# Optimization experiments

Hardware: AMD Instinct MI355X
Metric: run time of the kernel (lower is better)

Reference implementation:

```python
import jax, jax.numpy as jnp
import numpy as np

SIZE = 896   # hidden_size
HALF = 448   # hidden_size // 2
BINS = 256   # 2 ** (bits / 2)
B, T = 32, 1024


def _scale(x):
    # [0, BINS-1] ints -> [-1, 1] floats
    return x.astype(jnp.float32) / ((BINS - 1) / 2.0) - 1.0


def _reorder(w):
    # torch GRU layout (r, u, e) each split coarse/fine ->
    # (coarse_r, coarse_u, coarse_e, fine_r, fine_u, fine_e)
    cr, fr, cu, fu, ce, fe = jnp.split(w, 6, axis=0)
    return jnp.concatenate([cr, cu, ce, fr, fu, fe], axis=0)


def setup_inputs():
    key = jax.random.key(0)
    ks = jax.random.split(key, 14)
    s = 0.05
    return {
        'conditional': jax.random.normal(ks[0], (B, 3 * SIZE, T), jnp.float32) * s,
        'w_coarse_in': jax.random.normal(ks[1], (3 * HALF, 2), jnp.float32) * s,
        'w_fine_in': jax.random.normal(ks[2], (3 * HALF, 3), jnp.float32) * s,
        'w_hh': jax.random.normal(ks[3], (3 * SIZE, SIZE), jnp.float32) * s,
        'b_ih': jax.random.normal(ks[4], (3 * SIZE,), jnp.float32) * s,
        'b_hh': jax.random.normal(ks[5], (3 * SIZE,), jnp.float32) * s,
        'wc1': jax.random.normal(ks[6], (HALF, HALF), jnp.float32) * s,
        'bc1': jax.random.normal(ks[7], (HALF,), jnp.float32) * s,
        'wc2': jax.random.normal(ks[8], (BINS, HALF), jnp.float32) * s,
        'bc2': jax.random.normal(ks[9], (BINS,), jnp.float32) * s,
        'wf1': jax.random.normal(ks[10], (HALF, HALF), jnp.float32) * s,
        'bf1': jax.random.normal(ks[11], (HALF,), jnp.float32) * s,
        'wf2': jax.random.normal(ks[12], (BINS, HALF), jnp.float32) * s,
        'bf2': jax.random.normal(ks[13], (BINS,), jnp.float32) * s,
    }


def _gru_softmax_step(hid, ip, hp, W1, b1, W2, b2):
    # hid: [HALF, B]; ip, hp: [3*HALF, B]
    ru = jax.nn.sigmoid(hp[:2 * HALF] + ip[:2 * HALF])
    r, u = ru[:HALF], ru[HALF:]
    e = jnp.tanh(r * hp[2 * HALF:] + ip[2 * HALF:])
    hid = u * hid + (1.0 - u) * e
    h = jax.nn.relu(hid.T @ W1.T + b1)          # [B, HALF]
    logits = h @ W2.T + b2                       # [B, BINS]
    sample = jnp.argmax(logits, axis=1).astype(jnp.int32)  # argmax=True path
    return hid, sample


def reference(conditional, w_coarse_in, w_fine_in, w_hh, b_ih, b_hh,
              wc1, bc1, wc2, bc2, wf1, bf1, wf2, bf2):
    batch, _, sig_len = conditional.shape
    # [B, 3*SIZE, T] -> [B, T, 3, SIZE], add input bias, split coarse/fine halves
    cond = conditional.transpose(0, 2, 1).reshape(batch, sig_len, 3, SIZE)
    g = cond + b_ih.reshape(3, SIZE)
    # reshape keeps gate order (r, u, e) concatenated along last dim
    bias_c = g[..., :HALF].reshape(batch, sig_len, 3 * HALF).transpose(1, 2, 0)  # [T, 3H, B]
    bias_f = g[..., HALF:].reshape(batch, sig_len, 3 * HALF).transpose(1, 2, 0)

    w_hh_r = _reorder(w_hh)                 # [3*SIZE, SIZE]
    b_hh_r = _reorder(b_hh[:, None])        # [3*SIZE, 1]

    def step(carry, xs):
        coarse, fine, c_hid, f_hid = carry
        bc, bf = xs
        hidden = jnp.concatenate([c_hid, f_hid], axis=0)        # [SIZE, B]
        hp = w_hh_r @ hidden + b_hh_r                            # [3*SIZE, B]
        hp_c, hp_f = hp[:3 * HALF], hp[3 * HALF:]
        cin = jnp.stack([_scale(coarse), _scale(fine)], axis=1)  # [B, 2]
        c_hid, new_coarse = _gru_softmax_step(
            c_hid, w_coarse_in @ cin.T + bc, hp_c, wc1, bc1, wc2, bc2)
        fin = jnp.stack([_scale(coarse), _scale(fine), _scale(new_coarse)], axis=1)  # [B, 3]
        f_hid, new_fine = _gru_softmax_step(
            f_hid, w_fine_in @ fin.T + bf, hp_f, wf1, bf1, wf2, bf2)
        return (new_coarse, new_fine, c_hid, f_hid), (new_coarse, new_fine)

    init = (jnp.full((batch,), BINS // 2, jnp.int32),   # go coarse sample
            jnp.zeros((batch,), jnp.int32),              # go fine sample
            jnp.zeros((HALF, batch), jnp.float32),
            jnp.zeros((HALF, batch), jnp.float32))
    carry, (oc, of) = jax.lax.scan(step, init, (bias_c, bias_f))
    final_hidden = jnp.concatenate([carry[2], carry[3]], axis=0)  # [SIZE, B]
    return oc.T, of.T, final_hidden
```

## Files before the change

### kernel.cpp

```cpp
#include <hip/hip_runtime.h>
#include <math.h>


#define HALFN  448
#define SIZEN  896
#define RTOT   2688
#define NB     32
#define TSTEPS 1024
#define NWG    224
#define NTHR   512
#define CONDSTR (RTOT * TSTEPS)
#define RBN    28
#define FANIN  28

#define OFF_HID0  0
#define OFF_HID1  28672
#define OFF_H1TC  57344
#define OFF_H1TF  71680
#define OFF_NCP   86016
#define OFF_NFP   86080
#define OFF_DCTRC 86144
#define OFF_DCTRF 86176
#define OFF_FLAGS 86208

typedef unsigned long long u64t;

__device__ __forceinline__ int orig_row(int r) {
  int c = r / HALFN, o = r - c * HALFN;
  int oc = (c < 3) ? (2 * c) : (2 * (c - 3) + 1);
  return oc * HALFN + o;
}
__device__ __forceinline__ float sigm(float x) { return 1.0f / (1.0f + expf(-x)); }

__device__ __forceinline__ float gload(const float* p) {
  return __hip_atomic_load(const_cast<float*>(p), __ATOMIC_RELAXED, __HIP_MEMORY_SCOPE_AGENT);
}
__device__ __forceinline__ void gstore(float* p, float v) {
  __hip_atomic_store(p, v, __ATOMIC_RELAXED, __HIP_MEMORY_SCOPE_AGENT);
}
__device__ __forceinline__ u64t gload64(const u64t* p) {
  return __hip_atomic_load(const_cast<u64t*>(p), __ATOMIC_RELAXED, __HIP_MEMORY_SCOPE_AGENT);
}
__device__ __forceinline__ void gstore64(u64t* p, u64t v) {
  __hip_atomic_store(p, v, __ATOMIC_RELAXED, __HIP_MEMORY_SCOPE_AGENT);
}
__device__ __forceinline__ void gmax64(u64t* p, u64t v) {
  __hip_atomic_fetch_max(p, v, __ATOMIC_RELAXED, __HIP_MEMORY_SCOPE_AGENT);
}
__device__ __forceinline__ unsigned ctrload(const unsigned* p) {
  return __hip_atomic_load(const_cast<unsigned*>(p), __ATOMIC_RELAXED, __HIP_MEMORY_SCOPE_AGENT);
}
__device__ __forceinline__ unsigned f2ord(float f) {
  unsigned u = __float_as_uint(f);
  return (u & 0x80000000u) ? ~u : (u | 0x80000000u);
}

struct __align__(16) SM {
  float whh[12][SIZEN];
  float wc1l[2][HALFN];
  float wf1l[2][HALFN];
  float wc2l[10][HALFN];
  float wf2l[10][HALFN];
  float red[8][12][32];
  float condw[12][16][33];
  float h1c4[4][HALFN];
  float fcr[4][16][8];
  float flog[4][16];
  float hps[6][32];
  float hpfl[6][32];
  float chid[2][32];
  float fhid[2][32];
  float scvo[32], sfvo[32], sncn[32];
  float ncraw[32], nfraw[32];
  float wcil[2][3][2];
  float wfil[2][3][3];
  float bihl[12];
  float bhh_l[12];
  float bc2l[10], bf2l[10];
};

__device__ __forceinline__ void gridbar(unsigned* flags, unsigned ep, int& dead) {
  asm volatile("s_waitcnt vmcnt(0)" ::: "memory");
  __syncthreads();
  if (threadIdx.x == 0)
    __hip_atomic_store(&flags[blockIdx.x], ep, __ATOMIC_RELAXED, __HIP_MEMORY_SCOPE_AGENT);
  if (!dead) {
    int iters = 0;
    for (;;) {
      int ok = 1;
      if (threadIdx.x < NWG) {
        unsigned v = __hip_atomic_load(&flags[threadIdx.x], __ATOMIC_RELAXED, __HIP_MEMORY_SCOPE_AGENT);
        ok = (v >= ep) ? 1 : 0;
      }
      if (__syncthreads_and(ok)) break;
      if (++iters > (1 << 20)) { dead = 1; break; }
      __builtin_amdgcn_s_sleep(1);
    }
  } else {
    __syncthreads();
  }
}

__device__ __forceinline__ void pollmany(unsigned* arr, int n, unsigned target, int& dead) {
  if (!dead) {
    int it = 0;
    for (;;) {
      int ok = 1;
      if ((int)threadIdx.x < n)
        ok = (ctrload(&arr[threadIdx.x]) >= target) ? 1 : 0;
      if (__syncthreads_and(ok)) break;
      if (++it > (1 << 20)) { dead = 1; break; }
      __builtin_amdgcn_s_sleep(1);
    }
  } else {
    __syncthreads();
  }
}

extern "C" __global__ void wavernn_init(float* ws) {
  int i = blockIdx.x * blockDim.x + threadIdx.x;
  int st = gridDim.x * blockDim.x;
  for (int k = i; k < 2 * SIZEN * NB; k += st) ws[k] = 0.0f;
  if (i < 64) ((u64t*)(ws + OFF_NCP))[i] = 0ull;
  if (i < 64) ((unsigned*)(ws + OFF_DCTRC))[i] = 0u;
  if (i < 256) ((unsigned*)(ws + OFF_FLAGS))[i] = 0u;
}

extern "C" __global__ void __launch_bounds__(NTHR)
wavernn_persist(const float* __restrict__ cond,
                const float* __restrict__ wci, const float* __restrict__ wfi,
                const float* __restrict__ whh, const float* __restrict__ bih,
                const float* __restrict__ bhh,
                const float* __restrict__ wc1, const float* __restrict__ bc1,
                const float* __restrict__ wc2, const float* __restrict__ bc2,
                const float* __restrict__ wf1, const float* __restrict__ bf1,
                const float* __restrict__ wf2, const float* __restrict__ bf2,
                float* __restrict__ out, float* ws) {
  __shared__ SM sm;

  float* hid0 = ws + OFF_HID0;
  float* hid1 = ws + OFF_HID1;
  float* h1tc = ws + OFF_H1TC;
  float* h1tf = ws + OFF_H1TF;
  u64t*  ncp  = (u64t*)(ws + OFF_NCP);
  u64t*  nfp  = (u64t*)(ws + OFF_NFP);
  unsigned* dctrc = (unsigned*)(ws + OFF_DCTRC);
  unsigned* dctrf = (unsigned*)(ws + OFF_DCTRF);
  unsigned* flags = (unsigned*)(ws + OFF_FLAGS);

  const int w = blockIdx.x, tid = threadIdx.x;
  const int b = tid & 31, ks = tid >> 5;
  const int rb = w >> 3, bg = w & 7;
  const int fc2start = (rb < 4) ? rb * 10 : 40 + (rb - 4) * 9;
  const int fc2len   = (rb < 4) ? 10 : 9;
  unsigned ep = 0;
  int dead = 0;

#pragma unroll
  for (int rr = 0; rr < 12; rr++) {
    int R = (rr >> 1) * HALFN + 2 * w + (rr & 1);
    const float* src = whh + (size_t)orig_row(R) * SIZEN;
    for (int k = tid * 4; k < SIZEN; k += NTHR * 4)
      *(float4*)&sm.whh[rr][k] = *(const float4*)&src[k];
  }
  if (tid < 12) sm.bhh_l[tid] = bhh[orig_row((tid >> 1) * HALFN + 2 * w + (tid & 1))];
  for (int k = tid * 4; k < HALFN; k += NTHR * 4) {
    *(float4*)&sm.wc1l[0][k] = *(const float4*)&wc1[(size_t)(2 * w) * HALFN + k];
    *(float4*)&sm.wc1l[1][k] = *(const float4*)&wc1[(size_t)(2 * w + 1) * HALFN + k];
    *(float4*)&sm.wf1l[0][k] = *(const float4*)&wf1[(size_t)(2 * w) * HALFN + k];
    *(float4*)&sm.wf1l[1][k] = *(const float4*)&wf1[(size_t)(2 * w + 1) * HALFN + k];
  }
  for (int rr = 0; rr < fc2len; rr++) {
    for (int k = tid * 4; k < HALFN; k += NTHR * 4) {
      *(float4*)&sm.wc2l[rr][k] = *(const float4*)&wc2[(size_t)(fc2start + rr) * HALFN + k];
      *(float4*)&sm.wf2l[rr][k] = *(const float4*)&wf2[(size_t)(fc2start + rr) * HALFN + k];
    }
  }
  if (tid < fc2len) { sm.bc2l[tid] = bc2[fc2start + tid]; sm.bf2l[tid] = bf2[fc2start + tid]; }
  if (tid < 12) {
    int rk = tid;
    int R = ((rk >= 6) ? HALFN : 0) + ((rk % 6) >> 1) * SIZEN + 2 * w + (rk & 1);
    sm.bihl[rk] = bih[R];
  }
  if (tid < 2) {
    int j = 2 * w + tid;
#pragma unroll
    for (int g = 0; g < 3; g++) {
      sm.wcil[tid][g][0] = wci[(g * HALFN + j) * 2 + 0];
      sm.wcil[tid][g][1] = wci[(g * HALFN + j) * 2 + 1];
      sm.wfil[tid][g][0] = wfi[(g * HALFN + j) * 3 + 0];
      sm.wfil[tid][g][1] = wfi[(g * HALFN + j) * 3 + 1];
      sm.wfil[tid][g][2] = wfi[(g * HALFN + j) * 3 + 2];
    }
  }
  if (tid < 64) { sm.chid[tid >> 5][tid & 31] = 0.0f; sm.fhid[tid >> 5][tid & 31] = 0.0f; }
  if (tid < 32) { sm.scvo[tid] = 128.0f * (2.0f / 255.0f) - 1.0f; sm.sfvo[tid] = -1.0f; }
  __syncthreads();

  for (int t = 0; t < TSTEPS; ++t) {
    const float* hprev = (t & 1) ? hid0 : hid1;
    float*       hcur  = (t & 1) ? hid1 : hid0;
    const int tt = t & 15;

    {
      if (tt == 0) {
        for (int idx = tid; idx < 1536; idx += NTHR) {
          int rk = idx >> 7, rem = idx & 127;
          int bb = rem >> 2, part = rem & 3;
          int R = ((rk >= 6) ? HALFN : 0) + ((rk % 6) >> 1) * SIZEN + 2 * w + (rk & 1);
          float4 v = *(const float4*)&cond[(size_t)bb * CONDSTR + (size_t)R * TSTEPS + t + part * 4];
          sm.condw[rk][part * 4 + 0][bb] = v.x;
          sm.condw[rk][part * 4 + 1][bb] = v.y;
          sm.condw[rk][part * 4 + 2][bb] = v.z;
          sm.condw[rk][part * 4 + 3][bb] = v.w;
        }
      }

      float acc[12];
#pragma unroll
      for (int rr = 0; rr < 12; rr++) acc[rr] = 0.0f;
      const int k0 = ks * 56;
      const float* hcol = hprev + b;
#pragma unroll 2
      for (int k = k0; k < k0 + 56; k += 4) {
        float h0 = gload(&hcol[(k + 0) * 32]), h1v = gload(&hcol[(k + 1) * 32]);
        float h2 = gload(&hcol[(k + 2) * 32]), h3  = gload(&hcol[(k + 3) * 32]);
#pragma unroll
        for (int rr = 0; rr < 12; rr++) {
          const float4 wv = *(const float4*)&sm.whh[rr][k];
          acc[rr] = fmaf(wv.x, h0, fmaf(wv.y, h1v, fmaf(wv.z, h2, fmaf(wv.w, h3, acc[rr]))));
        }
      }
#pragma unroll
      for (int rr = 0; rr < 12; rr++) acc[rr] += __shfl_xor(acc[rr], 32);
      __syncthreads();
      if ((tid & 32) == 0) {
        int slot = ks >> 1;
#pragma unroll
        for (int rr = 0; rr < 12; rr++) sm.red[slot][rr][b] = acc[rr];
      }
      __syncthreads();
      if (tid < 384) {
        int rr = tid >> 5, bb = tid & 31;
        float s = sm.bhh_l[rr];
#pragma unroll
        for (int kk = 0; kk < 8; kk++) s += sm.red[kk][rr][bb];
        if (rr < 6) sm.hps[rr][bb] = s;
        else        sm.hpfl[rr - 6][bb] = s;
      }
      if (t > 0) {
        pollmany(dctrf, 32, FANIN * (unsigned)t, dead);
        if (tid < 32) {
          u64t p = gload64(&nfp[tid]);
          unsigned nf = 0xFFFFFFFFu - (unsigned)(p & 0xFFFFFFFFull);
          sm.sfvo[tid] = (float)nf * (2.0f / 255.0f) - 1.0f;
          sm.nfraw[tid] = (float)nf;
        }
      }
      __syncthreads();
      if (t > 0 && w < 32 && tid == 64)
        out[32768 + (size_t)w * TSTEPS + (t - 1)] = sm.nfraw[w];
      if (tid < 64) {
        int q = tid >> 5, bb = tid & 31;
        float sc = sm.scvo[bb], sf = sm.sfvo[bb];
        float ipr = sm.wcil[q][0][0] * sc + sm.wcil[q][0][1] * sf + sm.condw[0 + q][tt][bb] + sm.bihl[0 + q];
        float ipu = sm.wcil[q][1][0] * sc + sm.wcil[q][1][1] * sf + sm.condw[2 + q][tt][bb] + sm.bihl[2 + q];
        float ipe = sm.wcil[q][2][0] * sc + sm.wcil[q][2][1] * sf + sm.condw[4 + q][tt][bb] + sm.bihl[4 + q];
        float r = sigm(sm.hps[0 + q][bb] + ipr);
        float u = sigm(sm.hps[2 + q][bb] + ipu);
        float e = tanhf(fmaf(r, sm.hps[4 + q][bb], ipe));
        float hnew = u * sm.chid[q][bb] + (1.0f - u) * e;
        sm.chid[q][bb] = hnew;
        gstore(&hcur[(size_t)(2 * w + q) * 32 + bb], hnew);
      }
    }
    gridbar(flags, ++ep, dead);

    {
      const int k0 = ks * 28;
      float a0 = 0.0f, a1 = 0.0f;
      const float* hcc = hcur + b;
#pragma unroll
      for (int k = k0; k < k0 + 28; k += 4) {
        float h0 = gload(&hcc[(k + 0) * 32]), h1v = gload(&hcc[(k + 1) * 32]);
        float h2 = gload(&hcc[(k + 2) * 32]), h3  = gload(&hcc[(k + 3) * 32]);
        float4 v0 = *(const float4*)&sm.wc1l[0][k];
        a0 = fmaf(v0.x, h0, fmaf(v0.y, h1v, fmaf(v0.z, h2, fmaf(v0.w, h3, a0))));
        float4 v1 = *(const float4*)&sm.wc1l[1][k];
        a1 = fmaf(v1.x, h0, fmaf(v1.y, h1v, fmaf(v1.z, h2, fmaf(v1.w, h3, a1))));
      }
      a0 += __shfl_xor(a0, 32); a1 += __shfl_xor(a1, 32);
      __syncthreads();
      if ((tid & 32) == 0) { sm.red[ks >> 1][0][b] = a0; sm.red[ks >> 1][1][b] = a1; }
      if (w < 32 && tid == 256) gstore64(&nfp[w], 0ull);
      __syncthreads();
      if (tid < 64) {
        int rr = tid >> 5, bb = tid & 31;
        float s = bc1[2 * w + rr];
#pragma unroll
        for (int kk = 0; kk < 8; kk++) s += sm.red[kk][rr][bb];
        gstore(&h1tc[(size_t)bb * HALFN + 2 * w + rr], fmaxf(s, 0.0f));
      }
    }
    gridbar(flags, ++ep, dead);

    {
#pragma unroll
      for (int bq = 0; bq < 4; bq++)
        if (tid < HALFN) sm.h1c4[bq][tid] = gload(&h1tc[(size_t)(4 * bg + bq) * HALFN + tid]);
      __syncthreads();
      {
        int bq = tid >> 7, rl = (tid >> 3) & 15, kss = tid & 7;
        if (rl < fc2len) {
          const float* wrow = sm.wc2l[rl];
          const float* hcol = sm.h1c4[bq];
          float a = 0.0f;
          int kk0 = kss * 56;
#pragma unroll
          for (int k = kk0; k < kk0 + 56; k += 4) {
            float4 wv = *(const float4*)&wrow[k];
            float4 hv = *(const float4*)&hcol[k];
            a = fmaf(wv.x, hv.x, fmaf(wv.y, hv.y, fmaf(wv.z, hv.z, fmaf(wv.w, hv.w, a))));
          }
          sm.fcr[bq][rl][kss] = a;
        }
      }
      __syncthreads();
      if (tid < 64) {
        int bq = tid >> 4, rl = tid & 15;
        if (rl < fc2len) {
          float s = sm.bc2l[rl];
#pragma unroll
          for (int q = 0; q < 8; q++) s += sm.fcr[bq][rl][q];
          sm.flog[bq][rl] = s;
        }
      }
      __syncthreads();
      if (tid < 4) {
        int bq = tid;
        float bv = sm.flog[bq][0]; int bi = 0;
        for (int rl = 1; rl < fc2len; rl++) {
          float x = sm.flog[bq][rl];
          if (x > bv) { bv = x; bi = rl; }
        }
        u64t pack = ((u64t)f2ord(bv) << 32) | (u64t)(0xFFFFFFFFu - (unsigned)(fc2start + bi));
        gmax64(&ncp[4 * bg + bq], pack);
        asm volatile("s_waitcnt vmcnt(0)" ::: "memory");
        __hip_atomic_fetch_add(&dctrc[4 * bg + bq], 1u, __ATOMIC_RELAXED, __HIP_MEMORY_SCOPE_AGENT);
      }
    }
    pollmany(dctrc, 32, FANIN * (unsigned)(t + 1), dead);

    {
      if (tid < 32) {
        u64t p = gload64(&ncp[tid]);
        unsigned nc = 0xFFFFFFFFu - (unsigned)(p & 0xFFFFFFFFull);
        sm.sncn[tid] = (float)nc * (2.0f / 255.0f) - 1.0f;
        sm.ncraw[tid] = (float)nc;
      }
      __syncthreads();
      if (w < 32 && tid == 64) out[(size_t)w * TSTEPS + t] = sm.ncraw[w];
      if (tid < 64) {
        int q = tid >> 5, bb = tid & 31;
        float sc = sm.scvo[bb], sf = sm.sfvo[bb], snc = sm.sncn[bb];
        float ipr = sm.wfil[q][0][0] * sc + sm.wfil[q][0][1] * sf + sm.wfil[q][0][2] * snc
                  + sm.condw[6 + q][tt][bb] + sm.bihl[6 + q];
        float ipu = sm.wfil[q][1][0] * sc + sm.wfil[q][1][1] * sf + sm.wfil[q][1][2] * snc
                  + sm.condw[8 + q][tt][bb] + sm.bihl[8 + q];
        float ipe = sm.wfil[q][2][0] * sc + sm.wfil[q][2][1] * sf + sm.wfil[q][2][2] * snc
                  + sm.condw[10 + q][tt][bb] + sm.bihl[10 + q];
        float r = sigm(sm.hpfl[0 + q][bb] + ipr);
        float u = sigm(sm.hpfl[2 + q][bb] + ipu);
        float e = tanhf(fmaf(r, sm.hpfl[4 + q][bb], ipe));
        float hnew = u * sm.fhid[q][bb] + (1.0f - u) * e;
        sm.fhid[q][bb] = hnew;
        gstore(&hcur[(size_t)(HALFN + 2 * w + q) * 32 + bb], hnew);
      }
      __syncthreads();
      if (tid < 32) sm.scvo[tid] = sm.sncn[tid];
    }
    gridbar(flags, ++ep, dead);

    {
      const int k0 = ks * 28;
      float a0 = 0.0f, a1 = 0.0f;
      const float* hff = hcur + HALFN * 32 + b;
#pragma unroll
      for (int k = k0; k < k0 + 28; k += 4) {
        float h0 = gload(&hff[(k + 0) * 32]), h1v = gload(&hff[(k + 1) * 32]);
        float h2 = gload(&hff[(k + 2) * 32]), h3  = gload(&hff[(k + 3) * 32]);
        float4 v0 = *(const float4*)&sm.wf1l[0][k];
        a0 = fmaf(v0.x, h0, fmaf(v0.y, h1v, fmaf(v0.z, h2, fmaf(v0.w, h3, a0))));
        float4 v1 = *(const float4*)&sm.wf1l[1][k];
        a1 = fmaf(v1.x, h0, fmaf(v1.y, h1v, fmaf(v1.z, h2, fmaf(v1.w, h3, a1))));
      }
      a0 += __shfl_xor(a0, 32); a1 += __shfl_xor(a1, 32);
      __syncthreads();
      if ((tid & 32) == 0) { sm.red[ks >> 1][0][b] = a0; sm.red[ks >> 1][1][b] = a1; }
      if (w < 32 && tid == 256) gstore64(&ncp[w], 0ull);
      __syncthreads();
      if (tid < 64) {
        int rr = tid >> 5, bb = tid & 31;
        float s = bf1[2 * w + rr];
#pragma unroll
        for (int kk = 0; kk < 8; kk++) s += sm.red[kk][rr][bb];
        gstore(&h1tf[(size_t)bb * HALFN + 2 * w + rr], fmaxf(s, 0.0f));
      }
    }
    gridbar(flags, ++ep, dead);

    {
#pragma unroll
      for (int bq = 0; bq < 4; bq++)
        if (tid < HALFN) sm.h1c4[bq][tid] = gload(&h1tf[(size_t)(4 * bg + bq) * HALFN + tid]);
      __syncthreads();
      {
        int bq = tid >> 7, rl = (tid >> 3) & 15, kss = tid & 7;
        if (rl < fc2len) {
          const float* wrow = sm.wf2l[rl];
          const float* hcol = sm.h1c4[bq];
          float a = 0.0f;
          int kk0 = kss * 56;
#pragma unroll
          for (int k = kk0; k < kk0 + 56; k += 4) {
            float4 wv = *(const float4*)&wrow[k];
            float4 hv = *(const float4*)&hcol[k];
            a = fmaf(wv.x, hv.x, fmaf(wv.y, hv.y, fmaf(wv.z, hv.z, fmaf(wv.w, hv.w, a))));
          }
          sm.fcr[bq][rl][kss] = a;
        }
      }
      __syncthreads();
      if (tid < 64) {
        int bq = tid >> 4, rl = tid & 15;
        if (rl < fc2len) {
          float s = sm.bf2l[rl];
#pragma unroll
          for (int q = 0; q < 8; q++) s += sm.fcr[bq][rl][q];
          sm.flog[bq][rl] = s;
        }
      }
      __syncthreads();
      if (tid < 4) {
        int bq = tid;
        float bv = sm.flog[bq][0]; int bi = 0;
        for (int rl = 1; rl < fc2len; rl++) {
          float x = sm.flog[bq][rl];
          if (x > bv) { bv = x; bi = rl; }
        }
        u64t pack = ((u64t)f2ord(bv) << 32) | (u64t)(0xFFFFFFFFu - (unsigned)(fc2start + bi));
        gmax64(&nfp[4 * bg + bq], pack);
        asm volatile("s_waitcnt vmcnt(0)" ::: "memory");
        __hip_atomic_fetch_add(&dctrf[4 * bg + bq], 1u, __ATOMIC_RELAXED, __HIP_MEMORY_SCOPE_AGENT);
      }
    }
  }

  pollmany(dctrf, 32, FANIN * (unsigned)TSTEPS, dead);
  if (w < 32 && tid == 0) {
    u64t p = gload64(&nfp[w]);
    unsigned nf = 0xFFFFFFFFu - (unsigned)(p & 0xFFFFFFFFull);
    out[32768 + (size_t)w * TSTEPS + (TSTEPS - 1)] = (float)nf;
  }
  if (tid < 64) {
    int q = tid >> 5, bb = tid & 31;
    out[65536 + (size_t)(2 * w + q) * 32 + bb]         = sm.chid[q][bb];
    out[65536 + (size_t)(HALFN + 2 * w + q) * 32 + bb] = sm.fhid[q][bb];
  }
}

extern "C" void kernel_launch(void* const* d_in, const int* in_sizes, int n_in,
                              void* d_out, int out_size, void* d_ws, size_t ws_size,
                              hipStream_t stream) {
  const float* cond = (const float*)d_in[0];
  const float* wci  = (const float*)d_in[1];
  const float* wfi  = (const float*)d_in[2];
  const float* whh  = (const float*)d_in[3];
  const float* bih  = (const float*)d_in[4];
  const float* bhh  = (const float*)d_in[5];
  const float* wc1  = (const float*)d_in[6];
  const float* bc1  = (const float*)d_in[7];
  const float* wc2  = (const float*)d_in[8];
  const float* bc2  = (const float*)d_in[9];
  const float* wf1  = (const float*)d_in[10];
  const float* bf1  = (const float*)d_in[11];
  const float* wf2  = (const float*)d_in[12];
  const float* bf2  = (const float*)d_in[13];
  float* out = (float*)d_out;
  float* ws  = (float*)d_ws;

  hipLaunchKernelGGL(wavernn_init, dim3(64), dim3(256), 0, stream, ws);
  hipLaunchKernelGGL(wavernn_persist, dim3(NWG), dim3(NTHR), 0, stream,
                     cond, wci, wfi, whh, bih, bhh,
                     wc1, bc1, wc2, bc2, wf1, bf1, wf2, bf2, out, ws);
}
```

Before: 31.50 ms.

## Overlap next-step hidden matvec with fine-sample wait and shrink barrier polling to one wave

Moves the recurrent W_hh·h matvec for step t+1 to the end of step t, right after the fine-GRU hidden update, so it runs before the poll for the fine sample instead of sitting on the critical path after it. The coarse-input partial sum that does not depend on the fine sample is also precomputed. Grid barrier and counter polling now use a single wave with __all instead of block-wide __syncthreads_and, and the FC2 weight rows in shared memory are padded to avoid LDS bank conflicts. This relies on the hidden state being complete for all workgroups before the next-step matvec starts, and it makes the control flow more complex.

```diff
diff --git a/kernel.cpp b/kernel.cpp
--- a/kernel.cpp
+++ b/kernel.cpp
@@ -10,8 +10,8 @@
 #define NWG    224
 #define NTHR   512
 #define CONDSTR (RTOT * TSTEPS)
-#define RBN    28
 #define FANIN  28
+#define FC2PAD 452
 
 #define OFF_HID0  0
 #define OFF_HID1  28672
@@ -59,8 +59,8 @@
   float whh[12][SIZEN];
   float wc1l[2][HALFN];
   float wf1l[2][HALFN];
-  float wc2l[10][HALFN];
-  float wf2l[10][HALFN];
+  float wc2l[10][FC2PAD];
+  float wf2l[10][FC2PAD];
   float red[8][12][32];
   float condw[12][16][33];
   float h1c4[4][HALFN];
@@ -68,6 +68,7 @@
   float flog[4][16];
   float hps[6][32];
   float hpfl[6][32];
+  float ip0c[6][32];
   float chid[2][32];
   float fhid[2][32];
   float scvo[32], sfvo[32], sncn[32];
@@ -84,37 +85,39 @@
   __syncthreads();
   if (threadIdx.x == 0)
     __hip_atomic_store(&flags[blockIdx.x], ep, __ATOMIC_RELAXED, __HIP_MEMORY_SCOPE_AGENT);
-  if (!dead) {
-    int iters = 0;
-    for (;;) {
-      int ok = 1;
-      if (threadIdx.x < NWG) {
-        unsigned v = __hip_atomic_load(&flags[threadIdx.x], __ATOMIC_RELAXED, __HIP_MEMORY_SCOPE_AGENT);
-        ok = (v >= ep) ? 1 : 0;
-      }
-      if (__syncthreads_and(ok)) break;
-      if (++iters > (1 << 20)) { dead = 1; break; }
-      __builtin_amdgcn_s_sleep(1);
-    }
-  } else {
-    __syncthreads();
-  }
-}
-
-__device__ __forceinline__ void pollmany(unsigned* arr, int n, unsigned target, int& dead) {
-  if (!dead) {
+  if (threadIdx.x < 64 && !dead) {
     int it = 0;
     for (;;) {
       int ok = 1;
-      if ((int)threadIdx.x < n)
-        ok = (ctrload(&arr[threadIdx.x]) >= target) ? 1 : 0;
-      if (__syncthreads_and(ok)) break;
+#pragma unroll
+      for (int q = 0; q < 4; q++) {
+        int idx = (int)threadIdx.x + q * 64;
+        if (idx < NWG) {
+          unsigned v = __hip_atomic_load(&flags[idx], __ATOMIC_RELAXED, __HIP_MEMORY_SCOPE_AGENT);
+          ok &= (v >= ep) ? 1 : 0;
+        }
+      }
+      if (__all(ok)) break;
       if (++it > (1 << 20)) { dead = 1; break; }
       __builtin_amdgcn_s_sleep(1);
     }
-  } else {
-    __syncthreads();
-  }
+  }
+  __syncthreads();
+}
+
+__device__ __forceinline__ void pollmany(unsigned* arr, unsigned target, int& dead) {
+  if (threadIdx.x < 64 && !dead) {
+    int it = 0;
+    for (;;) {
+      int ok = 1;
+      if (threadIdx.x < 32)
+        ok = (ctrload(&arr[threadIdx.x]) >= target) ? 1 : 0;
+      if (__all(ok)) break;
+      if (++it > (1 << 20)) { dead = 1; break; }
+      __builtin_amdgcn_s_sleep(1);
+    }
+  }
+  __syncthreads();
 }
 
 extern "C" __global__ void wavernn_init(float* ws) {
@@ -197,59 +200,40 @@
   if (tid < 32) { sm.scvo[tid] = 128.0f * (2.0f / 255.0f) - 1.0f; sm.sfvo[tid] = -1.0f; }
   __syncthreads();
 
+  {
+    for (int idx = tid; idx < 1536; idx += NTHR) {
+      int rk = idx >> 7, rem = idx & 127;
+      int bb = rem >> 2, part = rem & 3;
+      int R = ((rk >= 6) ? HALFN : 0) + ((rk % 6) >> 1) * SIZEN + 2 * w + (rk & 1);
+      float4 v = *(const float4*)&cond[(size_t)bb * CONDSTR + (size_t)R * TSTEPS + 0 + part * 4];
+      sm.condw[rk][part * 4 + 0][bb] = v.x;
+      sm.condw[rk][part * 4 + 1][bb] = v.y;
+      sm.condw[rk][part * 4 + 2][bb] = v.z;
+      sm.condw[rk][part * 4 + 3][bb] = v.w;
+    }
+    __syncthreads();
+    if (tid < 384) {
+      int rr = tid >> 5, bb = tid & 31;
+      float s = sm.bhh_l[rr];
+      if (rr < 6) sm.hps[rr][bb] = s;
+      else        sm.hpfl[rr - 6][bb] = s;
+    }
+    if (tid < 192) {
+      int g2 = tid >> 5, bb = tid & 31;
+      int q = g2 & 1, g = g2 >> 1;
+      sm.ip0c[g2][bb] = sm.wcil[q][g][0] * sm.scvo[bb] + sm.condw[g2][0][bb] + sm.bihl[g2];
+    }
+    __syncthreads();
+  }
+
   for (int t = 0; t < TSTEPS; ++t) {
-    const float* hprev = (t & 1) ? hid0 : hid1;
+    const float* hcurG = (t & 1) ? hid1 : hid0;
     float*       hcur  = (t & 1) ? hid1 : hid0;
     const int tt = t & 15;
 
     {
-      if (tt == 0) {
-        for (int idx = tid; idx < 1536; idx += NTHR) {
-          int rk = idx >> 7, rem = idx & 127;
-          int bb = rem >> 2, part = rem & 3;
-          int R = ((rk >= 6) ? HALFN : 0) + ((rk % 6) >> 1) * SIZEN + 2 * w + (rk & 1);
-          float4 v = *(const float4*)&cond[(size_t)bb * CONDSTR + (size_t)R * TSTEPS + t + part * 4];
-          sm.condw[rk][part * 4 + 0][bb] = v.x;
-          sm.condw[rk][part * 4 + 1][bb] = v.y;
-          sm.condw[rk][part * 4 + 2][bb] = v.z;
-          sm.condw[rk][part * 4 + 3][bb] = v.w;
-        }
-      }
-
-      float acc[12];
-#pragma unroll
-      for (int rr = 0; rr < 12; rr++) acc[rr] = 0.0f;
-      const int k0 = ks * 56;
-      const float* hcol = hprev + b;
-#pragma unroll 2
-      for (int k = k0; k < k0 + 56; k += 4) {
-        float h0 = gload(&hcol[(k + 0) * 32]), h1v = gload(&hcol[(k + 1) * 32]);
-        float h2 = gload(&hcol[(k + 2) * 32]), h3  = gload(&hcol[(k + 3) * 32]);
-#pragma unroll
-        for (int rr = 0; rr < 12; rr++) {
-          const float4 wv = *(const float4*)&sm.whh[rr][k];
-          acc[rr] = fmaf(wv.x, h0, fmaf(wv.y, h1v, fmaf(wv.z, h2, fmaf(wv.w, h3, acc[rr]))));
-        }
-      }
-#pragma unroll
-      for (int rr = 0; rr < 12; rr++) acc[rr] += __shfl_xor(acc[rr], 32);
-      __syncthreads();
-      if ((tid & 32) == 0) {
-        int slot = ks >> 1;
-#pragma unroll
-        for (int rr = 0; rr < 12; rr++) sm.red[slot][rr][b] = acc[rr];
-      }
-      __syncthreads();
-      if (tid < 384) {
-        int rr = tid >> 5, bb = tid & 31;
-        float s = sm.bhh_l[rr];
-#pragma unroll
-        for (int kk = 0; kk < 8; kk++) s += sm.red[kk][rr][bb];
-        if (rr < 6) sm.hps[rr][bb] = s;
-        else        sm.hpfl[rr - 6][bb] = s;
-      }
       if (t > 0) {
-        pollmany(dctrf, 32, FANIN * (unsigned)t, dead);
+        pollmany(dctrf, FANIN * (unsigned)t, dead);
         if (tid < 32) {
           u64t p = gload64(&nfp[tid]);
           unsigned nf = 0xFFFFFFFFu - (unsigned)(p & 0xFFFFFFFFull);
@@ -262,10 +246,10 @@
         out[32768 + (size_t)w * TSTEPS + (t - 1)] = sm.nfraw[w];
       if (tid < 64) {
         int q = tid >> 5, bb = tid & 31;
-        float sc = sm.scvo[bb], sf = sm.sfvo[bb];
-        float ipr = sm.wcil[q][0][0] * sc + sm.wcil[q][0][1] * sf + sm.condw[0 + q][tt][bb] + sm.bihl[0 + q];
-        float ipu = sm.wcil[q][1][0] * sc + sm.wcil[q][1][1] * sf + sm.condw[2 + q][tt][bb] + sm.bihl[2 + q];
-        float ipe = sm.wcil[q][2][0] * sc + sm.wcil[q][2][1] * sf + sm.condw[4 + q][tt][bb] + sm.bihl[4 + q];
+        float sf = sm.sfvo[bb];
+        float ipr = sm.ip0c[0 + q][bb] + sm.wcil[q][0][1] * sf;
+        float ipu = sm.ip0c[2 + q][bb] + sm.wcil[q][1][1] * sf;
+        float ipe = sm.ip0c[4 + q][bb] + sm.wcil[q][2][1] * sf;
         float r = sigm(sm.hps[0 + q][bb] + ipr);
         float u = sigm(sm.hps[2 + q][bb] + ipu);
         float e = tanhf(fmaf(r, sm.hps[4 + q][bb], ipe));
@@ -349,7 +333,7 @@
         __hip_atomic_fetch_add(&dctrc[4 * bg + bq], 1u, __ATOMIC_RELAXED, __HIP_MEMORY_SCOPE_AGENT);
       }
     }
-    pollmany(dctrc, 32, FANIN * (unsigned)(t + 1), dead);
+    pollmany(dctrc, FANIN * (unsigned)(t + 1), dead);
 
     {
       if (tid < 32) {
@@ -454,9 +438,63 @@
         __hip_atomic_fetch_add(&dctrf[4 * bg + bq], 1u, __ATOMIC_RELAXED, __HIP_MEMORY_SCOPE_AGENT);
       }
     }
-  }
-
-  pollmany(dctrf, 32, FANIN * (unsigned)TSTEPS, dead);
+
+    if (t + 1 < TSTEPS) {
+      const int tn = t + 1, ttn = tn & 15;
+      if (ttn == 0) {
+        __syncthreads();
+        for (int idx = tid; idx < 1536; idx += NTHR) {
+          int rk = idx >> 7, rem = idx & 127;
+          int bb = rem >> 2, part = rem & 3;
+          int R = ((rk >= 6) ? HALFN : 0) + ((rk % 6) >> 1) * SIZEN + 2 * w + (rk & 1);
+          float4 v = *(const float4*)&cond[(size_t)bb * CONDSTR + (size_t)R * TSTEPS + tn + part * 4];
+          sm.condw[rk][part * 4 + 0][bb] = v.x;
+          sm.condw[rk][part * 4 + 1][bb] = v.y;
+          sm.condw[rk][part * 4 + 2][bb] = v.z;
+          sm.condw[rk][part * 4 + 3][bb] = v.w;
+        }
+      }
+      float acc[12];
+#pragma unroll
+      for (int rr = 0; rr < 12; rr++) acc[rr] = 0.0f;
+      const int k0 = ks * 56;
+      const float* hcol = hcurG + b;
+#pragma unroll 2
+      for (int k = k0; k < k0 + 56; k += 4) {
+        float h0 = gload(&hcol[(k + 0) * 32]), h1v = gload(&hcol[(k + 1) * 32]);
+        float h2 = gload(&hcol[(k + 2) * 32]), h3  = gload(&hcol[(k + 3) * 32]);
+#pragma unroll
+        for (int rr = 0; rr < 12; rr++) {
+          const float4 wv = *(const float4*)&sm.whh[rr][k];
+          acc[rr] = fmaf(wv.x, h0, fmaf(wv.y, h1v, fmaf(wv.z, h2, fmaf(wv.w, h3, acc[rr]))));
+        }
+      }
+#pragma unroll
+      for (int rr = 0; rr < 12; rr++) acc[rr] += __shfl_xor(acc[rr], 32);
+      __syncthreads();
+      if ((tid & 32) == 0) {
+        int slot = ks >> 1;
+#pragma unroll
+        for (int rr = 0; rr < 12; rr++) sm.red[slot][rr][b] = acc[rr];
+      }
+      __syncthreads();
+      if (tid < 384) {
+        int rr = tid >> 5, bb = tid & 31;
+        float s = sm.bhh_l[rr];
+#pragma unroll
+        for (int kk = 0; kk < 8; kk++) s += sm.red[kk][rr][bb];
+        if (rr < 6) sm.hps[rr][bb] = s;
+        else        sm.hpfl[rr - 6][bb] = s;
+      }
+      if (tid < 192) {
+        int g2 = tid >> 5, bb = tid & 31;
+        int q = g2 & 1, g = g2 >> 1;
+        sm.ip0c[g2][bb] = sm.wcil[q][g][0] * sm.scvo[bb] + sm.condw[g2][ttn][bb] + sm.bihl[g2];
+      }
+    }
+  }
+
+  pollmany(dctrf, FANIN * (unsigned)TSTEPS, dead);
   if (w < 32 && tid == 0) {
     u64t p = gload64(&nfp[w]);
     unsigned nf = 0xFFFFFFFFu - (unsigned)(p & 0xFFFFFFFFull);
```

New measurement: 33.13 ms. 1.05x slower.

## Double workgroup threads, halve per-thread K slices, single-wave barrier polling

Applied to the files above, without the earlier changes.

Raises the persistent kernel's block size from 512 to 1024 threads. Each thread now handles 28-element K slices in the recurrent matvec and the output-layer dot products, with 16-way reductions instead of 8. To make room in LDS, the second-layer weights and biases are no longer cached in shared memory and are read from global memory instead. Grid barriers and counter polls now spin in a single wave using __all instead of block-wide __syncthreads_and, which cuts per-iteration polling sync cost but adds global weight reads on the fc2 path.

```diff
diff --git a/kernel.cpp b/kernel.cpp
--- a/kernel.cpp
+++ b/kernel.cpp
@@ -8,9 +8,8 @@
 #define NB     32
 #define TSTEPS 1024
 #define NWG    224
-#define NTHR   512
+#define NTHR   1024
 #define CONDSTR (RTOT * TSTEPS)
-#define RBN    28
 #define FANIN  28
 
 #define OFF_HID0  0
@@ -59,12 +58,10 @@
   float whh[12][SIZEN];
   float wc1l[2][HALFN];
   float wf1l[2][HALFN];
-  float wc2l[10][HALFN];
-  float wf2l[10][HALFN];
-  float red[8][12][32];
+  float red[16][12][32];
   float condw[12][16][33];
   float h1c4[4][HALFN];
-  float fcr[4][16][8];
+  float fcr[4][16][16];
   float flog[4][16];
   float hps[6][32];
   float hpfl[6][32];
@@ -76,7 +73,6 @@
   float wfil[2][3][3];
   float bihl[12];
   float bhh_l[12];
-  float bc2l[10], bf2l[10];
 };
 
 __device__ __forceinline__ void gridbar(unsigned* flags, unsigned ep, int& dead) {
@@ -84,37 +80,39 @@
   __syncthreads();
   if (threadIdx.x == 0)
     __hip_atomic_store(&flags[blockIdx.x], ep, __ATOMIC_RELAXED, __HIP_MEMORY_SCOPE_AGENT);
-  if (!dead) {
-    int iters = 0;
-    for (;;) {
-      int ok = 1;
-      if (threadIdx.x < NWG) {
-        unsigned v = __hip_atomic_load(&flags[threadIdx.x], __ATOMIC_RELAXED, __HIP_MEMORY_SCOPE_AGENT);
-        ok = (v >= ep) ? 1 : 0;
-      }
-      if (__syncthreads_and(ok)) break;
-      if (++iters > (1 << 20)) { dead = 1; break; }
-      __builtin_amdgcn_s_sleep(1);
-    }
-  } else {
-    __syncthreads();
-  }
-}
-
-__device__ __forceinline__ void pollmany(unsigned* arr, int n, unsigned target, int& dead) {
-  if (!dead) {
+  if (threadIdx.x < 64 && !dead) {
     int it = 0;
     for (;;) {
       int ok = 1;
-      if ((int)threadIdx.x < n)
-        ok = (ctrload(&arr[threadIdx.x]) >= target) ? 1 : 0;
-      if (__syncthreads_and(ok)) break;
+#pragma unroll
+      for (int q = 0; q < 4; q++) {
+        int idx = (int)threadIdx.x + q * 64;
+        if (idx < NWG) {
+          unsigned v = __hip_atomic_load(&flags[idx], __ATOMIC_RELAXED, __HIP_MEMORY_SCOPE_AGENT);
+          ok &= (v >= ep) ? 1 : 0;
+        }
+      }
+      if (__all(ok)) break;
       if (++it > (1 << 20)) { dead = 1; break; }
       __builtin_amdgcn_s_sleep(1);
     }
-  } else {
-    __syncthreads();
-  }
+  }
+  __syncthreads();
+}
+
+__device__ __forceinline__ void pollmany(unsigned* arr, unsigned target, int& dead) {
+  if (threadIdx.x < 64 && !dead) {
+    int it = 0;
+    for (;;) {
+      int ok = 1;
+      if (threadIdx.x < 32)
+        ok = (ctrload(&arr[threadIdx.x]) >= target) ? 1 : 0;
+      if (__all(ok)) break;
+      if (++it > (1 << 20)) { dead = 1; break; }
+      __builtin_amdgcn_s_sleep(1);
+    }
+  }
+  __syncthreads();
 }
 
 extern "C" __global__ void wavernn_init(float* ws) {
@@ -170,13 +168,6 @@
     *(float4*)&sm.wf1l[0][k] = *(const float4*)&wf1[(size_t)(2 * w) * HALFN + k];
     *(float4*)&sm.wf1l[1][k] = *(const float4*)&wf1[(size_t)(2 * w + 1) * HALFN + k];
   }
-  for (int rr = 0; rr < fc2len; rr++) {
-    for (int k = tid * 4; k < HALFN; k += NTHR * 4) {
-      *(float4*)&sm.wc2l[rr][k] = *(const float4*)&wc2[(size_t)(fc2start + rr) * HALFN + k];
-      *(float4*)&sm.wf2l[rr][k] = *(const float4*)&wf2[(size_t)(fc2start + rr) * HALFN + k];
-    }
-  }
-  if (tid < fc2len) { sm.bc2l[tid] = bc2[fc2start + tid]; sm.bf2l[tid] = bf2[fc2start + tid]; }
   if (tid < 12) {
     int rk = tid;
     int R = ((rk >= 6) ? HALFN : 0) + ((rk % 6) >> 1) * SIZEN + 2 * w + (rk & 1);
@@ -219,10 +210,10 @@
       float acc[12];
 #pragma unroll
       for (int rr = 0; rr < 12; rr++) acc[rr] = 0.0f;
-      const int k0 = ks * 56;
+      const int k0 = ks * 28;
       const float* hcol = hprev + b;
-#pragma unroll 2
-      for (int k = k0; k < k0 + 56; k += 4) {
+#pragma unroll
+      for (int k = k0; k < k0 + 28; k += 4) {
         float h0 = gload(&hcol[(k + 0) * 32]), h1v = gload(&hcol[(k + 1) * 32]);
         float h2 = gload(&hcol[(k + 2) * 32]), h3  = gload(&hcol[(k + 3) * 32]);
 #pragma unroll
@@ -244,12 +235,12 @@
         int rr = tid >> 5, bb = tid & 31;
         float s = sm.bhh_l[rr];
 #pragma unroll
-        for (int kk = 0; kk < 8; kk++) s += sm.red[kk][rr][bb];
+        for (int kk = 0; kk < 16; kk++) s += sm.red[kk][rr][bb];
         if (rr < 6) sm.hps[rr][bb] = s;
         else        sm.hpfl[rr - 6][bb] = s;
       }
       if (t > 0) {
-        pollmany(dctrf, 32, FANIN * (unsigned)t, dead);
+        pollmany(dctrf, FANIN * (unsigned)t, dead);
         if (tid < 32) {
           u64t p = gload64(&nfp[tid]);
           unsigned nf = 0xFFFFFFFFu - (unsigned)(p & 0xFFFFFFFFull);
@@ -277,22 +268,24 @@
     gridbar(flags, ++ep, dead);
 
     {
-      const int k0 = ks * 28;
       float a0 = 0.0f, a1 = 0.0f;
-      const float* hcc = hcur + b;
-#pragma unroll
-      for (int k = k0; k < k0 + 28; k += 4) {
-        float h0 = gload(&hcc[(k + 0) * 32]), h1v = gload(&hcc[(k + 1) * 32]);
-        float h2 = gload(&hcc[(k + 2) * 32]), h3  = gload(&hcc[(k + 3) * 32]);
-        float4 v0 = *(const float4*)&sm.wc1l[0][k];
-        a0 = fmaf(v0.x, h0, fmaf(v0.y, h1v, fmaf(v0.z, h2, fmaf(v0.w, h3, a0))));
-        float4 v1 = *(const float4*)&sm.wc1l[1][k];
-        a1 = fmaf(v1.x, h0, fmaf(v1.y, h1v, fmaf(v1.z, h2, fmaf(v1.w, h3, a1))));
-      }
-      a0 += __shfl_xor(a0, 32); a1 += __shfl_xor(a1, 32);
-      __syncthreads();
-      if ((tid & 32) == 0) { sm.red[ks >> 1][0][b] = a0; sm.red[ks >> 1][1][b] = a1; }
-      if (w < 32 && tid == 256) gstore64(&nfp[w], 0ull);
+      if (ks < 16) {
+        const int k0 = ks * 28;
+        const float* hcc = hcur + b;
+#pragma unroll
+        for (int k = k0; k < k0 + 28; k += 4) {
+          float h0 = gload(&hcc[(k + 0) * 32]), h1v = gload(&hcc[(k + 1) * 32]);
+          float h2 = gload(&hcc[(k + 2) * 32]), h3  = gload(&hcc[(k + 3) * 32]);
+          float4 v0 = *(const float4*)&sm.wc1l[0][k];
+          a0 = fmaf(v0.x, h0, fmaf(v0.y, h1v, fmaf(v0.z, h2, fmaf(v0.w, h3, a0))));
+          float4 v1 = *(const float4*)&sm.wc1l[1][k];
+          a1 = fmaf(v1.x, h0, fmaf(v1.y, h1v, fmaf(v1.z, h2, fmaf(v1.w, h3, a1))));
+        }
+        a0 += __shfl_xor(a0, 32); a1 += __shfl_xor(a1, 32);
+      }
+      __syncthreads();
+      if (ks < 16 && (tid & 32) == 0) { sm.red[ks >> 1][0][b] = a0; sm.red[ks >> 1][1][b] = a1; }
+      if (w < 32 && tid == 512) gstore64(&nfp[w], 0ull);
       __syncthreads();
       if (tid < 64) {
         int rr = tid >> 5, bb = tid & 31;
@@ -305,19 +298,18 @@
     gridbar(flags, ++ep, dead);
 
     {
-#pragma unroll
-      for (int bq = 0; bq < 4; bq++)
-        if (tid < HALFN) sm.h1c4[bq][tid] = gload(&h1tc[(size_t)(4 * bg + bq) * HALFN + tid]);
+      for (int i = tid; i < 4 * HALFN; i += NTHR)
+        sm.h1c4[i / HALFN][i % HALFN] = gload(&h1tc[(size_t)(4 * bg + i / HALFN) * HALFN + (i % HALFN)]);
       __syncthreads();
       {
-        int bq = tid >> 7, rl = (tid >> 3) & 15, kss = tid & 7;
+        int bq = tid >> 8, rl = (tid >> 4) & 15, kss = tid & 15;
         if (rl < fc2len) {
-          const float* wrow = sm.wc2l[rl];
+          const float* wrow = wc2 + (size_t)(fc2start + rl) * HALFN;
           const float* hcol = sm.h1c4[bq];
           float a = 0.0f;
-          int kk0 = kss * 56;
-#pragma unroll
-          for (int k = kk0; k < kk0 + 56; k += 4) {
+          int kk0 = kss * 28;
+#pragma unroll
+          for (int k = kk0; k < kk0 + 28; k += 4) {
             float4 wv = *(const float4*)&wrow[k];
             float4 hv = *(const float4*)&hcol[k];
             a = fmaf(wv.x, hv.x, fmaf(wv.y, hv.y, fmaf(wv.z, hv.z, fmaf(wv.w, hv.w, a))));
@@ -329,9 +321,9 @@
       if (tid < 64) {
         int bq = tid >> 4, rl = tid & 15;
         if (rl < fc2len) {
-          float s = sm.bc2l[rl];
-#pragma unroll
-          for (int q = 0; q < 8; q++) s += sm.fcr[bq][rl][q];
+          float s = bc2[fc2start + rl];
+#pragma unroll
+          for (int q = 0; q < 16; q++) s += sm.fcr[bq][rl][q];
           sm.flog[bq][rl] = s;
         }
       }
@@ -349,7 +341,7 @@
         __hip_atomic_fetch_add(&dctrc[4 * bg + bq], 1u, __ATOMIC_RELAXED, __HIP_MEMORY_SCOPE_AGENT);
       }
     }
-    pollmany(dctrc, 32, FANIN * (unsigned)(t + 1), dead);
+    pollmany(dctrc, FANIN * (unsigned)(t + 1), dead);
 
     {
       if (tid < 32) {
@@ -382,22 +374,24 @@
     gridbar(flags, ++ep, dead);
 
     {
-      const int k0 = ks * 28;
       float a0 = 0.0f, a1 = 0.0f;
-      const float* hff = hcur + HALFN * 32 + b;
-#pragma unroll
-      for (int k = k0; k < k0 + 28; k += 4) {
-        float h0 = gload(&hff[(k + 0) * 32]), h1v = gload(&hff[(k + 1) * 32]);
-        float h2 = gload(&hff[(k + 2) * 32]), h3  = gload(&hff[(k + 3) * 32]);
-        float4 v0 = *(const float4*)&sm.wf1l[0][k];
-        a0 = fmaf(v0.x, h0, fmaf(v0.y, h1v, fmaf(v0.z, h2, fmaf(v0.w, h3, a0))));
-        float4 v1 = *(const float4*)&sm.wf1l[1][k];
-        a1 = fmaf(v1.x, h0, fmaf(v1.y, h1v, fmaf(v1.z, h2, fmaf(v1.w, h3, a1))));
-      }
-      a0 += __shfl_xor(a0, 32); a1 += __shfl_xor(a1, 32);
-      __syncthreads();
-      if ((tid & 32) == 0) { sm.red[ks >> 1][0][b] = a0; sm.red[ks >> 1][1][b] = a1; }
-      if (w < 32 && tid == 256) gstore64(&ncp[w], 0ull);
+      if (ks < 16) {
+        const int k0 = ks * 28;
+        const float* hff = hcur + HALFN * 32 + b;
+#pragma unroll
+        for (int k = k0; k < k0 + 28; k += 4) {
+          float h0 = gload(&hff[(k + 0) * 32]), h1v = gload(&hff[(k + 1) * 32]);
+          float h2 = gload(&hff[(k + 2) * 32]), h3  = gload(&hff[(k + 3) * 32]);
+          float4 v0 = *(const float4*)&sm.wf1l[0][k];
+          a0 = fmaf(v0.x, h0, fmaf(v0.y, h1v, fmaf(v0.z, h2, fmaf(v0.w, h3, a0))));
+          float4 v1 = *(const float4*)&sm.wf1l[1][k];
+          a1 = fmaf(v1.x, h0, fmaf(v1.y, h1v, fmaf(v1.z, h2, fmaf(v1.w, h3, a1))));
+        }
+        a0 += __shfl_xor(a0, 32); a1 += __shfl_xor(a1, 32);
+      }
+      __syncthreads();
+      if (ks < 16 && (tid & 32) == 0) { sm.red[ks >> 1][0][b] = a0; sm.red[ks >> 1][1][b] = a1; }
+      if (w < 32 && tid == 512) gstore64(&ncp[w], 0ull);
       __syncthreads();
       if (tid < 64) {
         int rr = tid >> 5, bb = tid & 31;
@@ -410,19 +404,18 @@
     gridbar(flags, ++ep, dead);
 
     {
-#pragma unroll
-      for (int bq = 0; bq < 4; bq++)
-        if (tid < HALFN) sm.h1c4[bq][tid] = gload(&h1tf[(size_t)(4 * bg + bq) * HALFN + tid]);
+      for (int i = tid; i < 4 * HALFN; i += NTHR)
+        sm.h1c4[i / HALFN][i % HALFN] = gload(&h1tf[(size_t)(4 * bg + i / HALFN) * HALFN + (i % HALFN)]);
       __syncthreads();
       {
-        int bq = tid >> 7, rl = (tid >> 3) & 15, kss = tid & 7;
+        int bq = tid >> 8, rl = (tid >> 4) & 15, kss = tid & 15;
         if (rl < fc2len) {
-          const float* wrow = sm.wf2l[rl];
+          const float* wrow = wf2 + (size_t)(fc2start + rl) * HALFN;
           const float* hcol = sm.h1c4[bq];
           float a = 0.0f;
-          int kk0 = kss * 56;
-#pragma unroll
-          for (int k = kk0; k < kk0 + 56; k += 4) {
+          int kk0 = kss * 28;
+#pragma unroll
+          for (int k = kk0; k < kk0 + 28; k += 4) {
             float4 wv = *(const float4*)&wrow[k];
             float4 hv = *(const float4*)&hcol[k];
             a = fmaf(wv.x, hv.x, fmaf(wv.y, hv.y, fmaf(wv.z, hv.z, fmaf(wv.w, hv.w, a))));
@@ -434,9 +427,9 @@
       if (tid < 64) {
         int bq = tid >> 4, rl = tid & 15;
         if (rl < fc2len) {
-          float s = sm.bf2l[rl];
-#pragma unroll
-          for (int q = 0; q < 8; q++) s += sm.fcr[bq][rl][q];
+          float s = bf2[fc2start + rl];
+#pragma unroll
+          for (int q = 0; q < 16; q++) s += sm.fcr[bq][rl][q];
           sm.flog[bq][rl] = s;
         }
       }
@@ -456,7 +449,7 @@
     }
   }
 
-  pollmany(dctrf, 32, FANIN * (unsigned)TSTEPS, dead);
+  pollmany(dctrf, FANIN * (unsigned)TSTEPS, dead);
   if (w < 32 && tid == 0) {
     u64t p = gload64(&nfp[w]);
     unsigned nf = 0xFFFFFFFFu - (unsigned)(p & 0xFFFFFFFFull);
```

After: 37.51 ms. 19.1% more time.
